# Performance work log

Measured on AMD Instinct MI355X. Metric: run time of the kernel, lower is better.

## Reference

```python
import jax, jax.numpy as jnp
import numpy as np

B, S, D = 2, 2048, 1024
R = 64
H = 16
DH = D // H
N = 32  # neurons per bank (fqk, fv, rqk, rv)


def setup_inputs() -> dict:
    key = jax.random.key(0)
    ks = jax.random.split(key, 13)
    inp = {
        'x': jax.random.normal(ks[0], (B, S, D), dtype=jnp.float32),
        'fqk_weights_Q': jax.random.uniform(ks[1], (B, S, N), dtype=jnp.float32),
        'fqk_weights_K': jax.random.uniform(ks[2], (B, S, N), dtype=jnp.float32),
        'fv_weights': jax.random.uniform(ks[3], (B, S, N), dtype=jnp.float32),
        'rqk_weights_Q': jax.random.uniform(ks[4], (B, S, N), dtype=jnp.float32),
        'rqk_weights_K': jax.random.uniform(ks[5], (B, S, N), dtype=jnp.float32),
        'rv_weights': jax.random.uniform(ks[6], (B, S, N), dtype=jnp.float32),
        # neuron banks (orthogonal init in original; random normal is fine for numerics)
        'f_qk': jax.random.normal(ks[7], (N, D, R), dtype=jnp.float32) / np.sqrt(D),
        'f_v': jax.random.normal(ks[8], (N, D, R), dtype=jnp.float32) / np.sqrt(D),
        'r_qk': jax.random.normal(ks[9], (N, R, D), dtype=jnp.float32) / np.sqrt(R),
        'r_v': jax.random.normal(ks[10], (N, R, D), dtype=jnp.float32) / np.sqrt(R),
        'W_O': jax.random.normal(ks[11], (D, D), dtype=jnp.float32) / np.sqrt(D),  # torch Linear weight [out,in]
    }
    return inp


def _mix_project(x, w, neurons):
    # h[b,s,r] = sum_n w[b,s,n] * (x[b,s,:] @ neurons[n])  -- reassociated, avoids [B,S,D,R]
    p = jnp.einsum('bsd,ndr->bsnr', x, neurons)  # [B,S,N,R]
    return jnp.einsum('bsn,bsnr->bsr', w, p)


def _mix_restore(h, w, neurons):
    # y[b,s,d] = sum_n w[b,s,n] * (h[b,s,:] @ neurons[n])  -- reassociated, avoids [B,S,R,D]
    hw = jnp.einsum('bsr,bsn->bsnr', h, w)  # [B,S,N,R]
    return jnp.einsum('bsnr,nrd->bsd', hw, neurons)


def _causal_sdpa(Q, K, V):
    # Q,K,V: [B,H,S,DH]
    scale = 1.0 / np.sqrt(Q.shape[-1]).astype(np.float32)
    scores = jnp.einsum('bhqd,bhkd->bhqk', Q, K) * scale
    s = Q.shape[2]
    mask = jnp.tril(jnp.ones((s, s), dtype=bool))
    scores = jnp.where(mask, scores, jnp.finfo(scores.dtype).min)
    attn = jax.nn.softmax(scores, axis=-1)
    return jnp.einsum('bhqk,bhkd->bhqd', attn, V)


def reference(x, fqk_weights_Q, fqk_weights_K, fv_weights,
              rqk_weights_Q, rqk_weights_K, rv_weights,
              f_qk, f_v, r_qk, r_v, W_O):
    b, s, d = x.shape
    h_q = _mix_project(x, fqk_weights_Q, f_qk)  # [B,S,R]
    h_k = _mix_project(x, fqk_weights_K, f_qk)
    h_v = _mix_project(x, fv_weights, f_v)

    Q = _mix_restore(h_q, rqk_weights_Q, r_qk)  # [B,S,D]
    K = _mix_restore(h_k, rqk_weights_K, r_qk)
    V = _mix_restore(h_v, rv_weights, r_v)

    Q = Q.reshape(b, s, H, DH).transpose(0, 2, 1, 3)
    K = K.reshape(b, s, H, DH).transpose(0, 2, 1, 3)
    V = V.reshape(b, s, H, DH).transpose(0, 2, 1, 3)

    attn_out = _causal_sdpa(Q, K, V)  # [B,H,S,DH]
    attn_out = attn_out.transpose(0, 2, 1, 3).reshape(b, s, d)
    out = attn_out @ W_O.T  # nn.Linear(d, d, bias=False)
    return out
```

## Files before the change

### kernel.cpp

```cpp
#include <hip/hip_runtime.h>
#include <hip/hip_bf16.h>
#include <cstdint>
#include <cstddef>

typedef unsigned short u16;
typedef short bfrag __attribute__((ext_vector_type(8)));
typedef _Float16 hfrag __attribute__((ext_vector_type(8)));
typedef float f32x4 __attribute__((ext_vector_type(4)));
typedef u16 u16x8 __attribute__((ext_vector_type(8)));

__device__ __forceinline__ u16 f2bf(float v) {
    union { float f; unsigned u; } a; a.f = v;
    unsigned r = a.u + 0x7fff + ((a.u >> 16) & 1);
    return (u16)(r >> 16);
}
__device__ __forceinline__ float bf2f(u16 u) {
    union { unsigned u; float f; } a; a.u = ((unsigned)u) << 16;
    return a.f;
}
__device__ __forceinline__ u16 f2h(float v) {
    union { _Float16 h; u16 u; } a; a.h = (_Float16)v;
    return a.u;
}
__device__ __forceinline__ f32x4 mfma_bf16(bfrag a, bfrag b, f32x4 c) {
    return __builtin_amdgcn_mfma_f32_16x16x32_bf16(a, b, c, 0, 0, 0);
}
__device__ __forceinline__ f32x4 mfma_f16(hfrag a, hfrag b, f32x4 c) {
    return __builtin_amdgcn_mfma_f32_16x16x32_f16(a, b, c, 0, 0, 0);
}
__device__ __forceinline__ void async_copy16(const void* g, void* l) {
    __builtin_amdgcn_global_load_lds(
        (const __attribute__((address_space(1))) unsigned*)g,
        (__attribute__((address_space(3))) unsigned*)l, 16, 0, 0);
}
__device__ __forceinline__ int get_xcd() {
    unsigned x;
    asm volatile("s_getreg_b32 %0, hwreg(HW_REG_XCC_ID)" : "=s"(x));
    return (int)(x & 7);
}

template<int SPLIT>
__global__ __launch_bounds__(256) void cast_split(const float* __restrict__ s,
                                                  u16* __restrict__ dh,
                                                  u16* __restrict__ dl, int n4)
{
    int i = blockIdx.x * 256 + threadIdx.x;
    if (i >= n4) return;
    float4 v = ((const float4*)s)[i];
    float vv[4] = {v.x, v.y, v.z, v.w};
    ushort4 h, l;
    u16* hp = (u16*)&h; u16* lp = (u16*)&l;
#pragma unroll
    for (int e = 0; e < 4; ++e) {
        u16 hb = f2bf(vv[e]);
        hp[e] = hb;
        if (SPLIT) lp[e] = f2bf(vv[e] - bf2f(hb));
    }
    ((ushort4*)dh)[i] = h;
    if (SPLIT) ((ushort4*)dl)[i] = l;
}

template<int MODE>
__global__ __launch_bounds__(256) void transpose_cast(const float* __restrict__ src,
                                                      u16* __restrict__ dh,
                                                      u16* __restrict__ dl,
                                                      int R, int C, int dpitch)
{
    __shared__ float t[32][33];
    int z = blockIdx.z;
    const float* s = src + (size_t)z * R * C;
    int r0 = blockIdx.y * 32, c0 = blockIdx.x * 32;
    int tx = threadIdx.x & 31, ty = threadIdx.x >> 5;
#pragma unroll
    for (int p = 0; p < 4; ++p)
        t[ty + p * 8][tx] = s[(size_t)(r0 + ty + p * 8) * C + c0 + tx];
    __syncthreads();
#pragma unroll
    for (int p = 0; p < 4; ++p) {
        int rr = ty + p * 8;
        float v = t[tx][rr];
        size_t di = (size_t)(z * C + c0 + rr) * dpitch + r0 + tx;
        if (MODE == 2) {
            dh[di] = f2h(v);
        } else {
            u16 hb = f2bf(v);
            dh[di] = hb;
            if (MODE == 1) dl[di] = f2bf(v - bf2f(hb));
        }
    }
}

template<int SPLIT, int CTH>
__global__ __launch_bounds__(256) void gemm_mfma(const u16* __restrict__ Agh,
                                                 const u16* __restrict__ Agl,
                                                 const u16* __restrict__ Bgh,
                                                 const u16* __restrict__ Bgl,
                                                 float* __restrict__ C,
                                                 int M, int N, int K)
{
    constexpr int HB = SPLIT ? 16384 : 8192;
    __shared__ u16 lds[2 * HB];

    const int bid = blockIdx.x;
    const int xq  = bid & 7;
    const int s   = bid >> 3;
    const int RP  = (M >> 7) >> 3;
    const int rowt = xq * RP + (s % RP);
    const int ct   = s / RP;
    const int row0 = rowt * 128;
    const int col0 = ct * 128;

    const int tid  = threadIdx.x;
    const int lane = tid & 63;
    const int wv   = tid >> 6;
    const int q    = lane >> 4;
    const int tn   = lane & 15;
    const int wm   = (wv >> 1) * 64;
    const int wn   = (wv & 1) * 64;
    const int wbase = (tid & 192) * 8;

    auto stage = [&](u16* base, int k0) {
        u16* Ath = base;
        u16* Atl = SPLIT ? (base + 4096) : base;
        u16* Bth = base + (SPLIT ? 8192 : 4096);
        u16* Btl = SPLIT ? (base + 12288) : base;
#pragma unroll
        for (int shot = 0; shot < 2; ++shot) {
            int G = tid + shot * 256;
            int row = G >> 2, kgs = G & 3;
            int kgg = kgs ^ ((row >> 1) & 3);
            size_t goffB = (size_t)(col0 + row) * K + k0 + kgg * 8;
            async_copy16(Bgh + goffB, Bth + shot * 2048 + wbase);
            if (SPLIT) async_copy16(Bgl + goffB, Btl + shot * 2048 + wbase);
            size_t goffA = (size_t)(row0 + row) * K + k0 + kgg * 8;
            async_copy16(Agh + goffA, Ath + shot * 2048 + wbase);
            if (SPLIT) async_copy16(Agl + goffA, Atl + shot * 2048 + wbase);
        }
    };

    f32x4 acc[4][4];
#pragma unroll
    for (int i = 0; i < 4; ++i)
#pragma unroll
        for (int j = 0; j < 4; ++j) acc[i][j] = 0.f;

    stage(lds, 0);
    __syncthreads();

    int cur = 0;
    const int NT = K >> 5;
    for (int n = 0; n < NT; ++n) {
        if (n + 1 < NT) stage(lds + (cur ^ 1) * HB, (n + 1) * 32);

        const u16* base = lds + cur * HB;
        const u16* Ath = base;
        const u16* Atl = SPLIT ? (base + 4096) : base;
        const u16* Bth = base + (SPLIT ? 8192 : 4096);
        const u16* Btl = SPLIT ? (base + 12288) : base;

        bfrag ah[4], bh[4], al[4], bl[4];
#pragma unroll
        for (int i = 0; i < 4; ++i) {
            int m = wm + i * 16 + tn;
            int g = m * 4 + (q ^ ((m >> 1) & 3));
            ah[i] = *(const bfrag*)(Ath + g * 8);
            if (SPLIT) al[i] = *(const bfrag*)(Atl + g * 8);
        }
#pragma unroll
        for (int j = 0; j < 4; ++j) {
            int n2 = wn + j * 16 + tn;
            int g = n2 * 4 + (q ^ ((n2 >> 1) & 3));
            bh[j] = *(const bfrag*)(Bth + g * 8);
            if (SPLIT) bl[j] = *(const bfrag*)(Btl + g * 8);
        }
#pragma unroll
        for (int i = 0; i < 4; ++i)
#pragma unroll
            for (int j = 0; j < 4; ++j) {
                acc[i][j] = mfma_bf16(ah[i], bh[j], acc[i][j]);
                if (SPLIT) {
                    acc[i][j] = mfma_bf16(ah[i], bl[j], acc[i][j]);
                    acc[i][j] = mfma_bf16(al[i], bh[j], acc[i][j]);
                }
            }
        __syncthreads();
        cur ^= 1;
    }

#pragma unroll
    for (int i = 0; i < 4; ++i)
#pragma unroll
        for (int j = 0; j < 4; ++j)
#pragma unroll
            for (int rg = 0; rg < 4; ++rg) {
                int row = row0 + wm + i * 16 + q * 4 + rg;
                int col = col0 + wn + j * 16 + tn;
                C[(size_t)row * N + col] = acc[i][j][rg];
            }
}

__global__ __launch_bounds__(256) void mix_ahw(const float* __restrict__ P,
                                               const float* __restrict__ wf1,
                                               const float* __restrict__ wr1,
                                               const float* __restrict__ wf2,
                                               const float* __restrict__ wr2,
                                               u16* __restrict__ A1,
                                               u16* __restrict__ A2,
                                               int two)
{
    __shared__ float sha[4][64], shb[4][64];
    const int tid = threadIdx.x;
    const int row = tid >> 6;
    const int r   = tid & 63;
    const int bs  = blockIdx.x * 4 + row;
    const float* Pp = P + (size_t)bs * 2048 + r;
    float a = 0.f, b = 0.f;
#pragma unroll
    for (int n = 0; n < 32; ++n) {
        float p = Pp[n * 64];
        a = fmaf(wf1[bs * 32 + n], p, a);
        if (two) b = fmaf(wf2[bs * 32 + n], p, b);
    }
    sha[row][r] = a;
    if (two) shb[row][r] = b;
    __syncthreads();

    const int n  = r >> 1;
    const int hf = (r & 1) * 32;
    const float wv1 = wr1[bs * 32 + n];
    const float wv2 = two ? wr2[bs * 32 + n] : 0.f;
    u16x8 o1[4], o2[4];
#pragma unroll
    for (int c = 0; c < 4; ++c)
#pragma unroll
        for (int e = 0; e < 8; ++e) {
            o1[c][e] = f2h(sha[row][hf + c * 8 + e] * wv1);
            if (two) o2[c][e] = f2h(shb[row][hf + c * 8 + e] * wv2);
        }
    size_t base = (size_t)bs * 2048 + r * 32;
#pragma unroll
    for (int c = 0; c < 4; ++c)
        *(u16x8*)(A1 + base + c * 8) = o1[c];
    if (two) {
#pragma unroll
        for (int c = 0; c < 4; ++c)
            *(u16x8*)(A2 + base + c * 8) = o2[c];
    }
}

__global__ __launch_bounds__(512) void restore_mega(
    const u16* __restrict__ AhwQ, const u16* __restrict__ AhwK,
    const u16* __restrict__ AhwV,
    const u16* __restrict__ Rqk, const u16* __restrict__ Rv,
    u16* __restrict__ Qf, u16* __restrict__ Kf, u16* __restrict__ Vt,
    int* __restrict__ queue)
{
    __shared__ int sjob;
    __shared__ u16 lds[8192];
    u16* Ath = lds;
    u16* Bth = lds + 4096;

    const int tid = threadIdx.x;
    if (tid == 0) {
        int xcd = get_xcd();
        int job = -1;
        for (int t = 0; t < 8; ++t) {
            int qi = (xcd + t) & 7;
            int j = atomicAdd(&queue[qi], 1);
            if (j < 96) { job = qi * 96 + j; break; }
        }
        sjob = job;
    }
    __syncthreads();
    const int job = sjob;
    if (job < 0) return;
    const int qi   = job / 96;
    const int j    = job % 96;
    const int p    = qi * 12 + (j >> 3);
    const int sel  = p >> 5;
    const int rowt = p & 31;
    const int ct   = j & 7;
    const u16* Ag = (sel == 0) ? AhwQ : (sel == 1) ? AhwK : AhwV;
    const u16* Bg = (sel < 2) ? Rqk : Rv;
    const int K = 2048;
    const int row0 = rowt * 128, col0 = ct * 128;

    const int lane = tid & 63;
    const int wv   = tid >> 6;
    const int q    = lane >> 4;
    const int tn   = lane & 15;
    const int wm   = (wv >> 1) * 32;
    const int wn   = (wv & 1) * 64;
    const int wbase = (tid & 0x1C0) * 8;

    const int grow = tid >> 2, kgs = tid & 3;
    const int kgg  = kgs ^ ((grow >> 1) & 3);

    f32x4 acc[2][4];
#pragma unroll
    for (int i = 0; i < 2; ++i)
#pragma unroll
        for (int jj2 = 0; jj2 < 4; ++jj2) acc[i][jj2] = 0.f;

    for (int k0 = 0; k0 < K; k0 += 32) {
        async_copy16(Bg + (size_t)(col0 + grow) * K + k0 + kgg * 8, Bth + wbase);
        async_copy16(Ag + (size_t)(row0 + grow) * K + k0 + kgg * 8, Ath + wbase);
        __syncthreads();

        hfrag ah[2], bh[4];
#pragma unroll
        for (int i = 0; i < 2; ++i) {
            int m = wm + i * 16 + tn;
            int g = m * 4 + (q ^ ((m >> 1) & 3));
            ah[i] = *(const hfrag*)(Ath + g * 8);
        }
#pragma unroll
        for (int jj2 = 0; jj2 < 4; ++jj2) {
            int n = wn + jj2 * 16 + tn;
            int g = n * 4 + (q ^ ((n >> 1) & 3));
            bh[jj2] = *(const hfrag*)(Bth + g * 8);
        }
#pragma unroll
        for (int i = 0; i < 2; ++i)
#pragma unroll
            for (int jj2 = 0; jj2 < 4; ++jj2)
                acc[i][jj2] = mfma_f16(ah[i], bh[jj2], acc[i][jj2]);
        __syncthreads();
    }

#pragma unroll
    for (int i = 0; i < 2; ++i)
#pragma unroll
        for (int jj2 = 0; jj2 < 4; ++jj2)
#pragma unroll
            for (int rg = 0; rg < 4; ++rg) {
                int row = row0 + wm + i * 16 + q * 4 + rg;
                int col = col0 + wn + jj2 * 16 + tn;
                float v = acc[i][jj2][rg];
                if (sel < 2) {
                    size_t ix = (((size_t)(row >> 11) * 16 + (col >> 6)) << 17)
                              | ((size_t)(row & 2047) << 6) | (size_t)(col & 63);
                    ((sel == 0) ? Qf : Kf)[ix] = f2h(v);
                } else {
                    size_t ix = ((((size_t)(row >> 11) * 16 + (col >> 6)) * 64
                                 + (size_t)(col & 63)) << 11) | (size_t)(row & 2047);
                    Vt[ix] = f2h(v);
                }
            }
}

template<int SHOTS>
__device__ __forceinline__ void stage_tile(u16* dst, const u16* src, int rowstride,
                                           int tid, int wuni)
{
#pragma unroll
    for (int shot = 0; shot < SHOTS; ++shot) {
        int sl = shot * 256 + tid;
        int m = sl >> 3, s = sl & 7, g = s ^ (m & 7);
        async_copy16(src + (size_t)m * rowstride + g * 8, dst + shot * 2048 + wuni);
    }
}

__global__ __launch_bounds__(256) void flash_part(const u16* __restrict__ Qf_g,
                                                  const u16* __restrict__ Kf_g,
                                                  const u16* __restrict__ Vt_g,
                                                  u16* __restrict__ Opart,
                                                  float* __restrict__ ml)
{
    const int bid = blockIdx.x;
    const int idx = bid >> 3;
    const int bh  = (bid & 7) + 8 * (idx & 3);
    const int rest = idx >> 2;
    const int qb = 31 - (rest >> 3);
    const int c  = rest & 7;
    const int g  = qb >> 2, rr = qb & 3;
    const int nch = g + 1;
    if (c >= nch) return;
    const int q0 = qb * 64;
    const int slot = bh * 144 + (qb + 2 * g * (g - 1) + rr * g) + c;

    const int tid = threadIdx.x;
    const int lane = tid & 63;
    const int wv = tid >> 6;
    const int q = lane >> 4;
    const int tn = lane & 15;
    const int wuni = (tid & 192) * 8;

    __shared__ u16 smem[20480];
    u16* sQ  = smem;
    u16* sK0 = smem + 4096;
    u16* sV0 = smem + 8192;
    u16* sV1 = smem + 12288;
    u16* sP  = smem + 16384;

    const size_t kbase = (size_t)bh * 2048 * 64;
    const size_t vbase = (size_t)bh * 64 * 2048;
    const int kt0    = 4 * c;
    const int kt_end = min(4 * c + 3, qb);

    const size_t qoff = ((size_t)bh * 2048 + q0) * 64;
    stage_tile<2>(sQ, Qf_g + qoff, 64, tid, wuni);
    stage_tile<2>(sK0, Kf_g + kbase + (size_t)(kt0 * 64) * 64, 64, tid, wuni);
    stage_tile<2>(sV0, Vt_g + vbase + kt0 * 64, 2048, tid, wuni);
    __syncthreads();

    hfrag qf[2];
#pragma unroll
    for (int ks = 0; ks < 2; ++ks) {
        int m = wv * 16 + tn;
        int slt = (ks * 4 + q) ^ (m & 7);
        qf[ks] = *(const hfrag*)(sQ + m * 64 + slt * 8);
    }
    __syncthreads();

    float m_i[4], l_i[4];
    f32x4 acc_o[4];
#pragma unroll
    for (int ri = 0; ri < 4; ++ri) { m_i[ri] = -3.0e38f; l_i[ri] = 0.f; }
#pragma unroll
    for (int dt = 0; dt < 4; ++dt) acc_o[dt] = 0.f;

    int cur = 0;
    for (int kt = kt0; kt <= kt_end; ++kt) {
        const u16* sK = cur ? sQ : sK0;
        const u16* sV = cur ? sV1 : sV0;
        if (kt < kt_end) {
            u16* nK = cur ? sK0 : sQ;
            u16* nV = cur ? sV0 : sV1;
            const int k1 = (kt + 1) * 64;
            stage_tile<2>(nK, Kf_g + kbase + (size_t)k1 * 64, 64, tid, wuni);
            stage_tile<2>(nV, Vt_g + vbase + k1, 2048, tid, wuni);
        }

        f32x4 accs[4];
#pragma unroll
        for (int n = 0; n < 4; ++n) accs[n] = 0.f;
#pragma unroll
        for (int n = 0; n < 4; ++n) {
            int r = n * 16 + tn;
#pragma unroll
            for (int ks = 0; ks < 2; ++ks) {
                int slt = (ks * 4 + q) ^ (r & 7);
                hfrag kf = *(const hfrag*)(sK + r * 64 + slt * 8);
                accs[n] = mfma_f16(qf[ks], kf, accs[n]);
            }
        }
        const bool diag = (kt == qb);
#pragma unroll
        for (int n = 0; n < 4; ++n)
#pragma unroll
            for (int ri = 0; ri < 4; ++ri) {
                float v = accs[n][ri] * 0.125f;
                if (diag && (n * 16 + tn > wv * 16 + q * 4 + ri)) v = -3.0e38f;
                accs[n][ri] = v;
            }
        float alpha[4], mnew[4], ssum[4];
#pragma unroll
        for (int ri = 0; ri < 4; ++ri) {
            float mx = fmaxf(fmaxf(accs[0][ri], accs[1][ri]),
                             fmaxf(accs[2][ri], accs[3][ri]));
#pragma unroll
            for (int xm = 1; xm < 16; xm <<= 1)
                mx = fmaxf(mx, __shfl_xor(mx, xm, 64));
            mnew[ri] = fmaxf(m_i[ri], mx);
            alpha[ri] = __expf(m_i[ri] - mnew[ri]);
            m_i[ri] = mnew[ri];
            ssum[ri] = 0.f;
        }
#pragma unroll
        for (int n = 0; n < 4; ++n)
#pragma unroll
            for (int ri = 0; ri < 4; ++ri) {
                float p = __expf(accs[n][ri] - mnew[ri]);
                ssum[ri] += p;
                int m = wv * 16 + q * 4 + ri;
                int cc = n * 16 + tn;
                int slt = (cc >> 3) ^ (m & 7);
                sP[m * 64 + slt * 8 + (cc & 7)] = f2h(p);
            }
#pragma unroll
        for (int ri = 0; ri < 4; ++ri) {
            float sm = ssum[ri];
#pragma unroll
            for (int xm = 1; xm < 16; xm <<= 1)
                sm += __shfl_xor(sm, xm, 64);
            l_i[ri] = l_i[ri] * alpha[ri] + sm;
#pragma unroll
            for (int dt = 0; dt < 4; ++dt) acc_o[dt][ri] *= alpha[ri];
        }
#pragma unroll
        for (int ks = 0; ks < 2; ++ks) {
            int m = wv * 16 + tn;
            int slt = (ks * 4 + q) ^ (m & 7);
            hfrag pf = *(const hfrag*)(sP + m * 64 + slt * 8);
#pragma unroll
            for (int dt = 0; dt < 4; ++dt) {
                int d = dt * 16 + tn;
                int vslt = (ks * 4 + q) ^ (d & 7);
                hfrag vf = *(const hfrag*)(sV + d * 64 + vslt * 8);
                acc_o[dt] = mfma_f16(pf, vf, acc_o[dt]);
            }
        }
        __syncthreads();
        cur ^= 1;
    }

#pragma unroll
    for (int dt = 0; dt < 4; ++dt)
#pragma unroll
        for (int ri = 0; ri < 4; ++ri) {
            int row = wv * 16 + q * 4 + ri;
            Opart[(size_t)slot * 4096 + row * 64 + dt * 16 + tn] = f2bf(acc_o[dt][ri]);
        }
    if (tn == 0) {
#pragma unroll
        for (int ri = 0; ri < 4; ++ri) {
            int row = wv * 16 + q * 4 + ri;
            ml[(size_t)slot * 128 + row]      = m_i[ri];
            ml[(size_t)slot * 128 + 64 + row] = l_i[ri];
        }
    }
}

__global__ __launch_bounds__(256) void flash_combine(const u16* __restrict__ Opart,
                                                     const float* __restrict__ ml,
                                                     u16* __restrict__ Am)
{
    const int qb = blockIdx.x, bh = blockIdx.y;
    const int g = qb >> 2, rr = qb & 3;
    const int nch = g + 1;
    const int base = bh * 144 + (qb + 2 * g * (g - 1) + rr * g);
    const int tid = threadIdx.x;
    const int row = tid >> 2;
    const int c0  = (tid & 3) * 16;

    float mstar = -3.0e38f;
    float mc[8];
#pragma unroll
    for (int c = 0; c < 8; ++c) {
        if (c < nch) {
            mc[c] = ml[(size_t)(base + c) * 128 + row];
            mstar = fmaxf(mstar, mc[c]);
        }
    }
    float lstar = 0.f, wc[8];
#pragma unroll
    for (int c = 0; c < 8; ++c) {
        if (c < nch) {
            wc[c] = __expf(mc[c] - mstar);
            lstar += ml[(size_t)(base + c) * 128 + 64 + row] * wc[c];
        }
    }
    float o[16];
#pragma unroll
    for (int j = 0; j < 16; ++j) o[j] = 0.f;
    for (int c = 0; c < nch; ++c) {
        const u16* p = Opart + (size_t)(base + c) * 4096 + row * 64 + c0;
        u16x8 v0 = *(const u16x8*)p;
        u16x8 v1 = *(const u16x8*)(p + 8);
#pragma unroll
        for (int j = 0; j < 8; ++j) {
            o[j]     = fmaf(bf2f(v0[j]), wc[c], o[j]);
            o[j + 8] = fmaf(bf2f(v1[j]), wc[c], o[j + 8]);
        }
    }
    float inv = 1.0f / lstar;
    int srow = qb * 64 + row;
    size_t obase = ((size_t)(bh >> 4) * 2048 + srow) * 1024
                 + (size_t)((bh & 15) * 64 + c0);
    u16x8 w0, w1;
#pragma unroll
    for (int j = 0; j < 8; ++j) {
        w0[j] = f2bf(o[j] * inv);
        w1[j] = f2bf(o[j + 8] * inv);
    }
    *(u16x8*)(Am + obase)     = w0;
    *(u16x8*)(Am + obase + 8) = w1;
}

extern "C" void kernel_launch(void* const* d_in, const int* in_sizes, int n_in,
                              void* d_out, int out_size, void* d_ws, size_t ws_size,
                              hipStream_t stream)
{
    const float* x     = (const float*)d_in[0];
    const float* wfqkQ = (const float*)d_in[1];
    const float* wfqkK = (const float*)d_in[2];
    const float* wfv   = (const float*)d_in[3];
    const float* wrqkQ = (const float*)d_in[4];
    const float* wrqkK = (const float*)d_in[5];
    const float* wrv   = (const float*)d_in[6];
    const float* f_qk  = (const float*)d_in[7];
    const float* f_v   = (const float*)d_in[8];
    const float* r_qk  = (const float*)d_in[9];
    const float* r_v   = (const float*)d_in[10];
    const float* W_O   = (const float*)d_in[11];
    float* out = (float*)d_out;

    const size_t MB = 1u << 20;
    char* w8 = (char*)d_ws;
    u16*  WOb   = (u16*)(w8 + 0);
    u16*  RqkT  = (u16*)(w8 + 2  * MB);
    u16*  RvT   = (u16*)(w8 + 6  * MB);
    u16*  x_hi  = (u16*)(w8 + 10 * MB);
    u16*  x_lo  = (u16*)(w8 + 18 * MB);
    u16*  FqkTh = (u16*)(w8 + 26 * MB);
    u16*  FqkTl = (u16*)(w8 + 30 * MB);
    u16*  FvT   = (u16*)(w8 + 34 * MB);
    u16*  AhwQ  = (u16*)(w8 + 10 * MB);
    u16*  AhwK  = (u16*)(w8 + 26 * MB);
    u16*  AhwV  = (u16*)(w8 + 42 * MB);
    float* P    = (float*)(w8 + 58 * MB);
    u16*  Qf    = (u16*)(w8 + 58 * MB);
    u16*  Kf    = (u16*)(w8 + 66 * MB);
    u16*  Vt    = (u16*)(w8 + 74 * MB);
    u16*  Opart = (u16*)(w8 + 10 * MB);
    float* mlws = (float*)(w8 + 46 * MB);
    u16*  Am    = (u16*)(w8 + 2  * MB);
    int*  queue = (int*)(w8 + 84 * MB);

    dim3 blk(256);

    cast_split<1><<<dim3(4096), blk, 0, stream>>>(x, x_hi, x_lo, 1024 * 1024);
    cast_split<0><<<dim3(1024), blk, 0, stream>>>(W_O, WOb, nullptr, 256 * 1024);
    transpose_cast<1><<<dim3(2, 32, 32), blk, 0, stream>>>(f_qk, FqkTh, FqkTl, 1024, 64, 1024);
    transpose_cast<0><<<dim3(2, 32, 32), blk, 0, stream>>>(f_v,  FvT,   nullptr, 1024, 64, 1024);
    transpose_cast<2><<<dim3(32, 64, 1), blk, 0, stream>>>(r_qk, RqkT, nullptr, 2048, 1024, 2048);
    transpose_cast<2><<<dim3(32, 64, 1), blk, 0, stream>>>(r_v,  RvT,  nullptr, 2048, 1024, 2048);

    gemm_mfma<0, 2><<<dim3(512), blk, 0, stream>>>(x_hi, nullptr, FvT, nullptr, P,
                                                   4096, 2048, 1024);
    mix_ahw<<<dim3(1024), blk, 0, stream>>>(P, wfv, wrv, nullptr, nullptr,
                                            AhwV, nullptr, 0);

    gemm_mfma<1, 2><<<dim3(512), blk, 0, stream>>>(x_hi, x_lo, FqkTh, FqkTl, P,
                                                   4096, 2048, 1024);
    mix_ahw<<<dim3(1024), blk, 0, stream>>>(P, wfqkQ, wrqkQ, wfqkK, wrqkK,
                                            AhwQ, AhwK, 1);

    hipMemsetAsync(queue, 0, 8 * sizeof(int), stream);
    restore_mega<<<dim3(768), dim3(512), 0, stream>>>(AhwQ, AhwK, AhwV, RqkT, RvT,
                                                      Qf, Kf, Vt, queue);

    flash_part<<<dim3(8192), blk, 0, stream>>>(Qf, Kf, Vt, Opart, mlws);
    flash_combine<<<dim3(32, 32), blk, 0, stream>>>(Opart, mlws, Am);

    gemm_mfma<0, 1><<<dim3(256), blk, 0, stream>>>(Am, nullptr, WOb, nullptr, out,
                                                   4096, 1024, 1024);
}
```

Before: 408.8 us.

## Build restore A-operand on the fly from h and routing weights inside restore GEMM

The mix kernel now writes only the small fp32 h vectors ([B,S,R]) and no longer materialises the expanded fp16 h*w operand ([B,S,N*R]) for Q, K and V. Inside restore_mega, each block keeps its rows of h in registers, stages the routing weights in LDS, and builds the A fragments by multiplying h by the per-neuron weight before each MFMA. This removes writing and re-reading roughly 48 MB of expanded operands, at the cost of extra VALU conversion work in the GEMM inner loop.

```diff
diff --git a/kernel.cpp b/kernel.cpp
--- a/kernel.cpp
+++ b/kernel.cpp
@@ -199,66 +199,39 @@
             }
 }
 
-__global__ __launch_bounds__(256) void mix_ahw(const float* __restrict__ P,
-                                               const float* __restrict__ wf1,
-                                               const float* __restrict__ wr1,
-                                               const float* __restrict__ wf2,
-                                               const float* __restrict__ wr2,
-                                               u16* __restrict__ A1,
-                                               u16* __restrict__ A2,
-                                               int two)
-{
-    __shared__ float sha[4][64], shb[4][64];
-    const int tid = threadIdx.x;
-    const int row = tid >> 6;
-    const int r   = tid & 63;
-    const int bs  = blockIdx.x * 4 + row;
+__global__ __launch_bounds__(256) void mix_kernel(const float* __restrict__ P,
+                                                  const float* __restrict__ w1,
+                                                  const float* __restrict__ w2,
+                                                  float* __restrict__ h1,
+                                                  float* __restrict__ h2,
+                                                  int two)
+{
+    int tid = blockIdx.x * 256 + threadIdx.x;
+    int bs = tid >> 6;
+    int r  = tid & 63;
     const float* Pp = P + (size_t)bs * 2048 + r;
     float a = 0.f, b = 0.f;
 #pragma unroll
     for (int n = 0; n < 32; ++n) {
         float p = Pp[n * 64];
-        a = fmaf(wf1[bs * 32 + n], p, a);
-        if (two) b = fmaf(wf2[bs * 32 + n], p, b);
-    }
-    sha[row][r] = a;
-    if (two) shb[row][r] = b;
-    __syncthreads();
-
-    const int n  = r >> 1;
-    const int hf = (r & 1) * 32;
-    const float wv1 = wr1[bs * 32 + n];
-    const float wv2 = two ? wr2[bs * 32 + n] : 0.f;
-    u16x8 o1[4], o2[4];
-#pragma unroll
-    for (int c = 0; c < 4; ++c)
-#pragma unroll
-        for (int e = 0; e < 8; ++e) {
-            o1[c][e] = f2h(sha[row][hf + c * 8 + e] * wv1);
-            if (two) o2[c][e] = f2h(shb[row][hf + c * 8 + e] * wv2);
-        }
-    size_t base = (size_t)bs * 2048 + r * 32;
-#pragma unroll
-    for (int c = 0; c < 4; ++c)
-        *(u16x8*)(A1 + base + c * 8) = o1[c];
-    if (two) {
-#pragma unroll
-        for (int c = 0; c < 4; ++c)
-            *(u16x8*)(A2 + base + c * 8) = o2[c];
-    }
+        a = fmaf(w1[bs * 32 + n], p, a);
+        if (two) b = fmaf(w2[bs * 32 + n], p, b);
+    }
+    h1[tid] = a;
+    if (two) h2[tid] = b;
 }
 
 __global__ __launch_bounds__(512) void restore_mega(
-    const u16* __restrict__ AhwQ, const u16* __restrict__ AhwK,
-    const u16* __restrict__ AhwV,
+    const float* __restrict__ hQ, const float* __restrict__ wQ,
+    const float* __restrict__ hK, const float* __restrict__ wK,
+    const float* __restrict__ hV, const float* __restrict__ wV,
     const u16* __restrict__ Rqk, const u16* __restrict__ Rv,
     u16* __restrict__ Qf, u16* __restrict__ Kf, u16* __restrict__ Vt,
     int* __restrict__ queue)
 {
     __shared__ int sjob;
-    __shared__ u16 lds[8192];
-    u16* Ath = lds;
-    u16* Bth = lds + 4096;
+    __shared__ u16 Blds[4096];
+    __shared__ float wsp[128 * 33];
 
     const int tid = threadIdx.x;
     if (tid == 0) {
@@ -280,7 +253,8 @@
     const int sel  = p >> 5;
     const int rowt = p & 31;
     const int ct   = j & 7;
-    const u16* Ag = (sel == 0) ? AhwQ : (sel == 1) ? AhwK : AhwV;
+    const float* hA = (sel == 0) ? hQ : (sel == 1) ? hK : hV;
+    const float* wA = (sel == 0) ? wQ : (sel == 1) ? wK : wV;
     const u16* Bg = (sel < 2) ? Rqk : Rv;
     const int K = 2048;
     const int row0 = rowt * 128, col0 = ct * 128;
@@ -293,6 +267,31 @@
     const int wn   = (wv & 1) * 64;
     const int wbase = (tid & 0x1C0) * 8;
 
+    {
+        const int m = tid >> 2, n0 = (tid & 3) * 8;
+        const float* wp = wA + (size_t)(row0 + m) * 32 + n0;
+        float4 a = *(const float4*)wp;
+        float4 b = *(const float4*)(wp + 4);
+        float* d = wsp + m * 33 + n0;
+        d[0] = a.x; d[1] = a.y; d[2] = a.z; d[3] = a.w;
+        d[4] = b.x; d[5] = b.y; d[6] = b.z; d[7] = b.w;
+    }
+
+    float hr[2][2][8];
+#pragma unroll
+    for (int i = 0; i < 2; ++i) {
+        const float* hp = hA + (size_t)(row0 + wm + i * 16 + tn) * 64 + q * 8;
+#pragma unroll
+        for (int sub = 0; sub < 2; ++sub) {
+            float4 v0 = *(const float4*)(hp + sub * 32);
+            float4 v1 = *(const float4*)(hp + sub * 32 + 4);
+            hr[i][sub][0] = v0.x; hr[i][sub][1] = v0.y;
+            hr[i][sub][2] = v0.z; hr[i][sub][3] = v0.w;
+            hr[i][sub][4] = v1.x; hr[i][sub][5] = v1.y;
+            hr[i][sub][6] = v1.z; hr[i][sub][7] = v1.w;
+        }
+    }
+
     const int grow = tid >> 2, kgs = tid & 3;
     const int kgg  = kgs ^ ((grow >> 1) & 3);
 
@@ -300,43 +299,54 @@
 #pragma unroll
     for (int i = 0; i < 2; ++i)
 #pragma unroll
-        for (int jj2 = 0; jj2 < 4; ++jj2) acc[i][jj2] = 0.f;
-
-    for (int k0 = 0; k0 < K; k0 += 32) {
-        async_copy16(Bg + (size_t)(col0 + grow) * K + k0 + kgg * 8, Bth + wbase);
-        async_copy16(Ag + (size_t)(row0 + grow) * K + k0 + kgg * 8, Ath + wbase);
-        __syncthreads();
-
-        hfrag ah[2], bh[4];
-#pragma unroll
-        for (int i = 0; i < 2; ++i) {
-            int m = wm + i * 16 + tn;
-            int g = m * 4 + (q ^ ((m >> 1) & 3));
-            ah[i] = *(const hfrag*)(Ath + g * 8);
-        }
-#pragma unroll
-        for (int jj2 = 0; jj2 < 4; ++jj2) {
-            int n = wn + jj2 * 16 + tn;
-            int g = n * 4 + (q ^ ((n >> 1) & 3));
-            bh[jj2] = *(const hfrag*)(Bth + g * 8);
-        }
+        for (int jj = 0; jj < 4; ++jj) acc[i][jj] = 0.f;
+
+    __syncthreads();
+
+    for (int kk = 0; kk < 32; ++kk) {
+        float wrv[2];
 #pragma unroll
         for (int i = 0; i < 2; ++i)
-#pragma unroll
-            for (int jj2 = 0; jj2 < 4; ++jj2)
-                acc[i][jj2] = mfma_f16(ah[i], bh[jj2], acc[i][jj2]);
-        __syncthreads();
+            wrv[i] = wsp[(wm + i * 16 + tn) * 33 + kk];
+
+#pragma unroll
+        for (int sub = 0; sub < 2; ++sub) {
+            const int k0 = kk * 64 + sub * 32;
+            async_copy16(Bg + (size_t)(col0 + grow) * K + k0 + kgg * 8,
+                         Blds + wbase);
+            __syncthreads();
+
+            hfrag bh[4];
+#pragma unroll
+            for (int jj = 0; jj < 4; ++jj) {
+                int n = wn + jj * 16 + tn;
+                int g = n * 4 + (q ^ ((n >> 1) & 3));
+                bh[jj] = *(const hfrag*)(Blds + g * 8);
+            }
+            hfrag af[2];
+#pragma unroll
+            for (int i = 0; i < 2; ++i)
+#pragma unroll
+                for (int e = 0; e < 8; ++e)
+                    af[i][e] = (_Float16)(hr[i][sub][e] * wrv[i]);
+#pragma unroll
+            for (int i = 0; i < 2; ++i)
+#pragma unroll
+                for (int jj = 0; jj < 4; ++jj)
+                    acc[i][jj] = mfma_f16(af[i], bh[jj], acc[i][jj]);
+            __syncthreads();
+        }
     }
 
 #pragma unroll
     for (int i = 0; i < 2; ++i)
 #pragma unroll
-        for (int jj2 = 0; jj2 < 4; ++jj2)
+        for (int jj = 0; jj < 4; ++jj)
 #pragma unroll
             for (int rg = 0; rg < 4; ++rg) {
                 int row = row0 + wm + i * 16 + q * 4 + rg;
-                int col = col0 + wn + jj2 * 16 + tn;
-                float v = acc[i][jj2][rg];
+                int col = col0 + wn + jj * 16 + tn;
+                float v = acc[i][jj][rg];
                 if (sel < 2) {
                     size_t ix = (((size_t)(row >> 11) * 16 + (col >> 6)) << 17)
                               | ((size_t)(row & 2047) << 6) | (size_t)(col & 63);
@@ -606,9 +616,9 @@
     u16*  FqkTh = (u16*)(w8 + 26 * MB);
     u16*  FqkTl = (u16*)(w8 + 30 * MB);
     u16*  FvT   = (u16*)(w8 + 34 * MB);
-    u16*  AhwQ  = (u16*)(w8 + 10 * MB);
-    u16*  AhwK  = (u16*)(w8 + 26 * MB);
-    u16*  AhwV  = (u16*)(w8 + 42 * MB);
+    float* h_q  = (float*)(w8 + 42 * MB);
+    float* h_k  = (float*)(w8 + 43 * MB);
+    float* h_v  = (float*)(w8 + 44 * MB);
     float* P    = (float*)(w8 + 58 * MB);
     u16*  Qf    = (u16*)(w8 + 58 * MB);
     u16*  Kf    = (u16*)(w8 + 66 * MB);
@@ -629,16 +639,15 @@
 
     gemm_mfma<0, 2><<<dim3(512), blk, 0, stream>>>(x_hi, nullptr, FvT, nullptr, P,
                                                    4096, 2048, 1024);
-    mix_ahw<<<dim3(1024), blk, 0, stream>>>(P, wfv, wrv, nullptr, nullptr,
-                                            AhwV, nullptr, 0);
+    mix_kernel<<<dim3(1024), blk, 0, stream>>>(P, wfv, nullptr, h_v, nullptr, 0);
 
     gemm_mfma<1, 2><<<dim3(512), blk, 0, stream>>>(x_hi, x_lo, FqkTh, FqkTl, P,
                                                    4096, 2048, 1024);
-    mix_ahw<<<dim3(1024), blk, 0, stream>>>(P, wfqkQ, wrqkQ, wfqkK, wrqkK,
-                                            AhwQ, AhwK, 1);
+    mix_kernel<<<dim3(1024), blk, 0, stream>>>(P, wfqkQ, wfqkK, h_q, h_k, 1);
 
     hipMemsetAsync(queue, 0, 8 * sizeof(int), stream);
-    restore_mega<<<dim3(768), dim3(512), 0, stream>>>(AhwQ, AhwK, AhwV, RqkT, RvT,
+    restore_mega<<<dim3(768), dim3(512), 0, stream>>>(h_q, wrqkQ, h_k, wrqkK,
+                                                      h_v, wrv, RqkT, RvT,
                                                       Qf, Kf, Vt, queue);
 
     flash_part<<<dim3(8192), blk, 0, stream>>>(Qf, Kf, Vt, Opart, mlws);
```

Result: faster. 394.5 us (-3.5%).
